# Performance work log

Hardware: AMD Instinct MI355X
Metric: run time of the kernel (lower is better)

The kernel has to match this reference:

```python
import jax, jax.numpy as jnp
import numpy as np

EPS = 1e-12  # torch F.normalize default eps


def _nn_idx(q, ref):
    # q: [P,3], ref: [M,3] -> nearest-ref index per query point (brute-force chamfer NN)
    d = (jnp.sum(q * q, axis=-1, keepdims=True)
         - 2.0 * (q @ ref.T)
         + jnp.sum(ref * ref, axis=-1))  # [P,M]
    return jnp.argmin(d, axis=-1)  # [P]


def _verts_normals(verts, faces):
    # verts: [N,3], faces: [F,3] int. Area-weighted vertex normals (pytorch3d style):
    # accumulate the face cross-product into each incident vertex.
    v0 = verts[faces[:, 0]]
    v1 = verts[faces[:, 1]]
    v2 = verts[faces[:, 2]]
    fn = jnp.cross(v1 - v0, v2 - v0)  # [F,3], magnitude = 2*area
    n = jnp.zeros_like(verts)
    n = n.at[faces[:, 0]].add(fn)
    n = n.at[faces[:, 1]].add(fn)
    n = n.at[faces[:, 2]].add(fn)
    return n  # [N,3] (unnormalized; normalized downstream)


def _normalize(x):
    nrm = jnp.linalg.norm(x, axis=-1, keepdims=True)
    return x / jnp.maximum(nrm, EPS)


def setup_inputs() -> dict:
    key = jax.random.key(0)
    k1, k2, k3, k4 = jax.random.split(key, 4)
    B, P, V, N, F = 8, 2048, 2562, 8192, 16384
    return {
        "pred_points": jax.random.normal(k1, (B, P, 3), dtype=jnp.float32),
        "pred_vertices": jax.random.normal(k2, (B, V, 3), dtype=jnp.float32),
        "gt_vertices": jax.random.normal(k3, (B, N, 3), dtype=jnp.float32),
        "gt_faces": jax.random.randint(k4, (B, F, 3), 0, N, dtype=jnp.int64),
    }


def reference(pred_points, pred_vertices, gt_vertices, gt_faces):
    # nearest gt vertex for every sampled pred point (per-batch chamfer NN)
    nearest_gt_idx = jax.vmap(_nn_idx)(pred_points, gt_vertices)       # [B,P]
    # nearest pred-mesh vertex for every sampled pred point
    nearest_pred_idx = jax.vmap(_nn_idx)(pred_points, pred_vertices)   # [B,P]

    # gather nearest pred vertices: [B,P,3]
    nearest_pred_vertices = jnp.take_along_axis(
        pred_vertices, nearest_pred_idx[..., None], axis=1)

    # gt vertex normals, gathered at nearest gt indices, then normalized
    gt_normals = jax.vmap(_verts_normals)(gt_vertices, gt_faces)       # [B,N,3]
    nearest_gt_normals = jnp.take_along_axis(
        gt_normals, nearest_gt_idx[..., None], axis=1)                 # [B,P,3]
    nearest_gt_normals = _normalize(nearest_gt_normals)

    # edge from nearest pred vertex to sampled point, normalized
    nearest_pred_edges = _normalize(pred_points - nearest_pred_vertices)

    normal_loss = jnp.mean(jnp.abs(
        jnp.sum(nearest_pred_edges * nearest_gt_normals, axis=2)))
    return normal_loss
```

## Files before the change

kernel.cpp:

```cpp
#include <hip/hip_runtime.h>
#include <math.h>

#define BB 8
#define PP 2048
#define VV 2562
#define NV 8192
#define FF 16384
#define EPSF 1e-12f

__global__ __launch_bounds__(256) void face_normals_kernel(
    const float* __restrict__ gtv,
    const int*   __restrict__ faces,
    float*       __restrict__ nrm)
{
    int t = blockIdx.x * blockDim.x + threadIdx.x;
    if (t >= BB * FF) return;
    int b = t / FF;
    const int* fc = faces + (size_t)t * 3;
    int i0 = fc[0], i1 = fc[1], i2 = fc[2];

    const float* vb = gtv + (size_t)b * NV * 3;
    float v0x = vb[i0*3+0], v0y = vb[i0*3+1], v0z = vb[i0*3+2];
    float v1x = vb[i1*3+0], v1y = vb[i1*3+1], v1z = vb[i1*3+2];
    float v2x = vb[i2*3+0], v2y = vb[i2*3+1], v2z = vb[i2*3+2];

    float e1x = v1x - v0x, e1y = v1y - v0y, e1z = v1z - v0z;
    float e2x = v2x - v0x, e2y = v2y - v0y, e2z = v2z - v0z;

    float fnx = e1y * e2z - e1z * e2y;
    float fny = e1z * e2x - e1x * e2z;
    float fnz = e1x * e2y - e1y * e2x;

    float* nb = nrm + (size_t)b * NV * 3;
    atomicAdd(&nb[i0*3+0], fnx); atomicAdd(&nb[i0*3+1], fny); atomicAdd(&nb[i0*3+2], fnz);
    atomicAdd(&nb[i1*3+0], fnx); atomicAdd(&nb[i1*3+1], fny); atomicAdd(&nb[i1*3+2], fnz);
    atomicAdd(&nb[i2*3+0], fnx); atomicAdd(&nb[i2*3+1], fny); atomicAdd(&nb[i2*3+2], fnz);
}

__global__ __launch_bounds__(256) void nn_loss_kernel(
    const float* __restrict__ pp,
    const float* __restrict__ pv,
    const float* __restrict__ gtv,
    const float* __restrict__ nrm,
    float*       __restrict__ partial)
{
    const int lane = threadIdx.x & 63;
    const int wave = threadIdx.x >> 6;
    const int gw   = blockIdx.x * 4 + wave;
    const int b    = gw >> 9;
    const int p0   = (gw & 511) * 4;

    float px[4], py[4], pz[4];
    const float* ppb = pp + ((size_t)b * PP + p0) * 3;
#pragma unroll
    for (int j = 0; j < 4; ++j) {
        px[j] = ppb[j*3+0]; py[j] = ppb[j*3+1]; pz[j] = ppb[j*3+2];
    }

    float bd[4]; int bi[4];
#pragma unroll
    for (int j = 0; j < 4; ++j) { bd[j] = INFINITY; bi[j] = 0; }

    const float* gvb = gtv + (size_t)b * NV * 3;
    for (int i = 0; i < NV / 64; ++i) {
        int r = lane + i * 64;
        float rx = gvb[r*3+0], ry = gvb[r*3+1], rz = gvb[r*3+2];
#pragma unroll
        for (int j = 0; j < 4; ++j) {
            float dx = px[j] - rx, dy = py[j] - ry, dz = pz[j] - rz;
            float d = fmaf(dx, dx, fmaf(dy, dy, dz * dz));
            bool take = d < bd[j];
            bd[j] = take ? d : bd[j];
            bi[j] = take ? r : bi[j];
        }
    }

    int gt_idx[4];
#pragma unroll
    for (int j = 0; j < 4; ++j) {
        float d = bd[j]; int idx = bi[j];
#pragma unroll
        for (int off = 32; off; off >>= 1) {
            float od = __shfl_xor(d, off);
            int   oi = __shfl_xor(idx, off);
            if (od < d || (od == d && oi < idx)) { d = od; idx = oi; }
        }
        gt_idx[j] = idx;
    }

#pragma unroll
    for (int j = 0; j < 4; ++j) { bd[j] = INFINITY; bi[j] = 0; }

    const float* pvb = pv + (size_t)b * VV * 3;
    for (int i = 0; i < (VV + 63) / 64; ++i) {
        int r = lane + i * 64;
        int rc = (r < VV) ? r : (VV - 1);
        float rx = pvb[rc*3+0], ry = pvb[rc*3+1], rz = pvb[rc*3+2];
#pragma unroll
        for (int j = 0; j < 4; ++j) {
            float dx = px[j] - rx, dy = py[j] - ry, dz = pz[j] - rz;
            float d = fmaf(dx, dx, fmaf(dy, dy, dz * dz));
            d = (r < VV) ? d : INFINITY;
            bool take = d < bd[j];
            bd[j] = take ? d : bd[j];
            bi[j] = take ? r : bi[j];
        }
    }

    int pr_idx[4];
#pragma unroll
    for (int j = 0; j < 4; ++j) {
        float d = bd[j]; int idx = bi[j];
#pragma unroll
        for (int off = 32; off; off >>= 1) {
            float od = __shfl_xor(d, off);
            int   oi = __shfl_xor(idx, off);
            if (od < d || (od == d && oi < idx)) { d = od; idx = oi; }
        }
        pr_idx[j] = idx;
    }

    __shared__ float wsum[4];
    if (lane == 0) {
        const float* nb = nrm + (size_t)b * NV * 3;
        float s = 0.f;
#pragma unroll
        for (int j = 0; j < 4; ++j) {
            int vi = pr_idx[j];
            float ex = px[j] - pvb[vi*3+0];
            float ey = py[j] - pvb[vi*3+1];
            float ez = pz[j] - pvb[vi*3+2];
            float el = fmaxf(sqrtf(fmaf(ex, ex, fmaf(ey, ey, ez * ez))), EPSF);

            int ni = gt_idx[j];
            float nx = nb[ni*3+0];
            float ny = nb[ni*3+1];
            float nz = nb[ni*3+2];
            float nl = fmaxf(sqrtf(fmaf(nx, nx, fmaf(ny, ny, nz * nz))), EPSF);

            float dot = fmaf(ex, nx, fmaf(ey, ny, ez * nz));
            s += fabsf(dot / (el * nl));
        }
        wsum[wave] = s;
    }
    __syncthreads();
    if (threadIdx.x == 0)
        partial[blockIdx.x] = wsum[0] + wsum[1] + wsum[2] + wsum[3];
}

__global__ __launch_bounds__(256) void reduce_kernel(
    const float* __restrict__ partial, float* __restrict__ out, int n)
{
    int t = threadIdx.x;
    float s = 0.f;
    for (int i = t; i < n; i += 256) s += partial[i];
#pragma unroll
    for (int off = 32; off; off >>= 1) s += __shfl_xor(s, off);
    __shared__ float ws[4];
    if ((t & 63) == 0) ws[t >> 6] = s;
    __syncthreads();
    if (t == 0) out[0] = (ws[0] + ws[1] + ws[2] + ws[3]) / (float)(BB * PP);
}

extern "C" void kernel_launch(void* const* d_in, const int* in_sizes, int n_in,
                              void* d_out, int out_size, void* d_ws, size_t ws_size,
                              hipStream_t stream) {
    const float* pp    = (const float*)d_in[0];
    const float* pv    = (const float*)d_in[1];
    const float* gtv   = (const float*)d_in[2];
    const int*   faces = (const int*)d_in[3];
    float* out = (float*)d_out;

    float* nrm     = (float*)d_ws;
    float* partial = (float*)((char*)d_ws + (size_t)BB*NV*3*sizeof(float));

    hipMemsetAsync(nrm, 0, (size_t)BB * NV * 3 * sizeof(float), stream);

    face_normals_kernel<<<(BB * FF + 255) / 256, 256, 0, stream>>>(gtv, faces, nrm);

    const int nblocks = (BB * PP) / 16;
    nn_loss_kernel<<<nblocks, 256, 0, stream>>>(pp, pv, gtv, nrm, partial);

    reduce_kernel<<<1, 256, 0, stream>>>(partial, out, nblocks);
}
```

Baseline: 177.8 us.

## Split NN search across two waves per point group and accumulate normals in LDS

The face-normal kernel now runs one 1024-thread block per batch and does its scatter-add into a 96KB shared-memory accumulator before writing out. That replaces the global atomics and the workspace memset, at the cost of using only 8 blocks. The NN kernel splits each reference set into halves handled by paired waves and merges the two results through shared memory. It uses the expanded distance form (rr - 2p·r) to save arithmetic and folds the final reduction into a global atomicAdd, which removes the reduce kernel. The split doubles the number of blocks for the NN search, while the 8-block normals kernel may underuse the GPU.

Result: slower. 294.2 us (+65.5%).

```diff
diff --git a/kernel.cpp b/kernel.cpp
--- a/kernel.cpp
+++ b/kernel.cpp
@@ -7,34 +7,45 @@
 #define NV 8192
 #define FF 16384
 #define EPSF 1e-12f
+#define HNV 4096
+#define HVV 1281
 
-__global__ __launch_bounds__(256) void face_normals_kernel(
+__global__ __launch_bounds__(1024) void face_normals_kernel(
     const float* __restrict__ gtv,
     const int*   __restrict__ faces,
     float*       __restrict__ nrm)
 {
-    int t = blockIdx.x * blockDim.x + threadIdx.x;
-    if (t >= BB * FF) return;
-    int b = t / FF;
-    const int* fc = faces + (size_t)t * 3;
-    int i0 = fc[0], i1 = fc[1], i2 = fc[2];
+    __shared__ float acc[NV * 3];
+    const int b = blockIdx.x;
 
-    const float* vb = gtv + (size_t)b * NV * 3;
-    float v0x = vb[i0*3+0], v0y = vb[i0*3+1], v0z = vb[i0*3+2];
-    float v1x = vb[i1*3+0], v1y = vb[i1*3+1], v1z = vb[i1*3+2];
-    float v2x = vb[i2*3+0], v2y = vb[i2*3+1], v2z = vb[i2*3+2];
+    for (int i = threadIdx.x; i < NV * 3; i += 1024) acc[i] = 0.f;
+    __syncthreads();
 
-    float e1x = v1x - v0x, e1y = v1y - v0y, e1z = v1z - v0z;
-    float e2x = v2x - v0x, e2y = v2y - v0y, e2z = v2z - v0z;
+    const int*   fb = faces + (size_t)b * FF * 3;
+    const float* vb = gtv   + (size_t)b * NV * 3;
 
-    float fnx = e1y * e2z - e1z * e2y;
-    float fny = e1z * e2x - e1x * e2z;
-    float fnz = e1x * e2y - e1y * e2x;
+    for (int f = threadIdx.x; f < FF; f += 1024) {
+        int i0 = fb[f*3+0], i1 = fb[f*3+1], i2 = fb[f*3+2];
+
+        float v0x = vb[i0*3+0], v0y = vb[i0*3+1], v0z = vb[i0*3+2];
+        float v1x = vb[i1*3+0], v1y = vb[i1*3+1], v1z = vb[i1*3+2];
+        float v2x = vb[i2*3+0], v2y = vb[i2*3+1], v2z = vb[i2*3+2];
+
+        float e1x = v1x - v0x, e1y = v1y - v0y, e1z = v1z - v0z;
+        float e2x = v2x - v0x, e2y = v2y - v0y, e2z = v2z - v0z;
+
+        float fnx = e1y * e2z - e1z * e2y;
+        float fny = e1z * e2x - e1x * e2z;
+        float fnz = e1x * e2y - e1y * e2x;
+
+        atomicAdd(&acc[i0*3+0], fnx); atomicAdd(&acc[i0*3+1], fny); atomicAdd(&acc[i0*3+2], fnz);
+        atomicAdd(&acc[i1*3+0], fnx); atomicAdd(&acc[i1*3+1], fny); atomicAdd(&acc[i1*3+2], fnz);
+        atomicAdd(&acc[i2*3+0], fnx); atomicAdd(&acc[i2*3+1], fny); atomicAdd(&acc[i2*3+2], fnz);
+    }
+    __syncthreads();
 
     float* nb = nrm + (size_t)b * NV * 3;
-    atomicAdd(&nb[i0*3+0], fnx); atomicAdd(&nb[i0*3+1], fny); atomicAdd(&nb[i0*3+2], fnz);
-    atomicAdd(&nb[i1*3+0], fnx); atomicAdd(&nb[i1*3+1], fny); atomicAdd(&nb[i1*3+2], fnz);
-    atomicAdd(&nb[i2*3+0], fnx); atomicAdd(&nb[i2*3+1], fny); atomicAdd(&nb[i2*3+2], fnz);
+    for (int i = threadIdx.x; i < NV * 3; i += 1024) nb[i] = acc[i];
 }
 
 __global__ __launch_bounds__(256) void nn_loss_kernel(
@@ -42,40 +53,48 @@
     const float* __restrict__ pv,
     const float* __restrict__ gtv,
     const float* __restrict__ nrm,
-    float*       __restrict__ partial)
+    float*       __restrict__ out)
 {
+    __shared__ float sdg[2][2][4];  __shared__ int sig[2][2][4];
+    __shared__ float sdp[2][2][4];  __shared__ int sip[2][2][4];
+
     const int lane = threadIdx.x & 63;
     const int wave = threadIdx.x >> 6;
-    const int gw   = blockIdx.x * 4 + wave;
-    const int b    = gw >> 9;
-    const int p0   = (gw & 511) * 4;
+    const int g    = wave >> 1;
+    const int h    = wave & 1;
+    const int b    = blockIdx.x >> 8;
+    const int pbase = (blockIdx.x & 255) * 8 + g * 4;
 
-    float px[4], py[4], pz[4];
-    const float* ppb = pp + ((size_t)b * PP + p0) * 3;
+    float m2x[4], m2y[4], m2z[4];
+    {
+        const float* ppb = pp + ((size_t)b * PP + pbase) * 3;
 #pragma unroll
-    for (int j = 0; j < 4; ++j) {
-        px[j] = ppb[j*3+0]; py[j] = ppb[j*3+1]; pz[j] = ppb[j*3+2];
+        for (int j = 0; j < 4; ++j) {
+            m2x[j] = -2.f * ppb[j*3+0];
+            m2y[j] = -2.f * ppb[j*3+1];
+            m2z[j] = -2.f * ppb[j*3+2];
+        }
     }
 
     float bd[4]; int bi[4];
+
 #pragma unroll
     for (int j = 0; j < 4; ++j) { bd[j] = INFINITY; bi[j] = 0; }
-
-    const float* gvb = gtv + (size_t)b * NV * 3;
-    for (int i = 0; i < NV / 64; ++i) {
-        int r = lane + i * 64;
-        float rx = gvb[r*3+0], ry = gvb[r*3+1], rz = gvb[r*3+2];
+    {
+        const float* gvb = gtv + ((size_t)b * NV + (size_t)h * HNV) * 3;
+        for (int i = 0; i < HNV / 64; ++i) {
+            int r = lane + i * 64;
+            float rx = gvb[r*3+0], ry = gvb[r*3+1], rz = gvb[r*3+2];
+            float rr = fmaf(rx, rx, fmaf(ry, ry, rz * rz));
 #pragma unroll
-        for (int j = 0; j < 4; ++j) {
-            float dx = px[j] - rx, dy = py[j] - ry, dz = pz[j] - rz;
-            float d = fmaf(dx, dx, fmaf(dy, dy, dz * dz));
-            bool take = d < bd[j];
-            bd[j] = take ? d : bd[j];
-            bi[j] = take ? r : bi[j];
+            for (int j = 0; j < 4; ++j) {
+                float s = fmaf(m2x[j], rx, fmaf(m2y[j], ry, fmaf(m2z[j], rz, rr)));
+                bool take = s < bd[j];
+                bd[j] = take ? s : bd[j];
+                bi[j] = take ? r : bi[j];
+            }
         }
     }
-
-    int gt_idx[4];
 #pragma unroll
     for (int j = 0; j < 4; ++j) {
         float d = bd[j]; int idx = bi[j];
@@ -85,29 +104,29 @@
             int   oi = __shfl_xor(idx, off);
             if (od < d || (od == d && oi < idx)) { d = od; idx = oi; }
         }
-        gt_idx[j] = idx;
+        if (lane == 0) { sdg[g][h][j] = d; sig[g][h][j] = idx + h * HNV; }
     }
 
 #pragma unroll
     for (int j = 0; j < 4; ++j) { bd[j] = INFINITY; bi[j] = 0; }
-
-    const float* pvb = pv + (size_t)b * VV * 3;
-    for (int i = 0; i < (VV + 63) / 64; ++i) {
-        int r = lane + i * 64;
-        int rc = (r < VV) ? r : (VV - 1);
-        float rx = pvb[rc*3+0], ry = pvb[rc*3+1], rz = pvb[rc*3+2];
+    {
+        const float* pvh = pv + ((size_t)b * VV + (size_t)h * HVV) * 3;
+        for (int i = 0; i < (HVV + 63) / 64; ++i) {
+            int r = lane + i * 64;
+            bool ok = r < HVV;
+            int rc = ok ? r : 0;
+            float rx = pvh[rc*3+0], ry = pvh[rc*3+1], rz = pvh[rc*3+2];
+            float rr = fmaf(rx, rx, fmaf(ry, ry, rz * rz));
 #pragma unroll
-        for (int j = 0; j < 4; ++j) {
-            float dx = px[j] - rx, dy = py[j] - ry, dz = pz[j] - rz;
-            float d = fmaf(dx, dx, fmaf(dy, dy, dz * dz));
-            d = (r < VV) ? d : INFINITY;
-            bool take = d < bd[j];
-            bd[j] = take ? d : bd[j];
-            bi[j] = take ? r : bi[j];
+            for (int j = 0; j < 4; ++j) {
+                float s = fmaf(m2x[j], rx, fmaf(m2y[j], ry, fmaf(m2z[j], rz, rr)));
+                s = ok ? s : INFINITY;
+                bool take = s < bd[j];
+                bd[j] = take ? s : bd[j];
+                bi[j] = take ? r : bi[j];
+            }
         }
     }
-
-    int pr_idx[4];
 #pragma unroll
     for (int j = 0; j < 4; ++j) {
         float d = bd[j]; int idx = bi[j];
@@ -117,49 +136,45 @@
             int   oi = __shfl_xor(idx, off);
             if (od < d || (od == d && oi < idx)) { d = od; idx = oi; }
         }
-        pr_idx[j] = idx;
+        if (lane == 0) { sdp[g][h][j] = d; sip[g][h][j] = idx + h * HVV; }
     }
 
-    __shared__ float wsum[4];
-    if (lane == 0) {
-        const float* nb = nrm + (size_t)b * NV * 3;
+    __syncthreads();
+
+    if (wave == 0) {
         float s = 0.f;
-#pragma unroll
-        for (int j = 0; j < 4; ++j) {
-            int vi = pr_idx[j];
-            float ex = px[j] - pvb[vi*3+0];
-            float ey = py[j] - pvb[vi*3+1];
-            float ez = pz[j] - pvb[vi*3+2];
+        if (lane < 8) {
+            int gg = lane >> 2, q = lane & 3;
+
+            float d0 = sdg[gg][0][q], d1 = sdg[gg][1][q];
+            int   i0 = sig[gg][0][q], i1 = sig[gg][1][q];
+            int gi = (d1 < d0 || (d1 == d0 && i1 < i0)) ? i1 : i0;
+
+            float e0 = sdp[gg][0][q], e1 = sdp[gg][1][q];
+            int   j0 = sip[gg][0][q], j1 = sip[gg][1][q];
+            int pi = (e1 < e0 || (e1 == e0 && j1 < j0)) ? j1 : j0;
+
+            int pidx = (blockIdx.x & 255) * 8 + lane;
+            const float* pq = pp + ((size_t)b * PP + pidx) * 3;
+            float px = pq[0], py = pq[1], pz = pq[2];
+
+            const float* pvr = pv + ((size_t)b * VV + pi) * 3;
+            float ex = px - pvr[0], ey = py - pvr[1], ez = pz - pvr[2];
             float el = fmaxf(sqrtf(fmaf(ex, ex, fmaf(ey, ey, ez * ez))), EPSF);
 
-            int ni = gt_idx[j];
-            float nx = nb[ni*3+0];
-            float ny = nb[ni*3+1];
-            float nz = nb[ni*3+2];
+            const float* nb = nrm + ((size_t)b * NV + gi) * 3;
+            float nx = nb[0], ny = nb[1], nz = nb[2];
             float nl = fmaxf(sqrtf(fmaf(nx, nx, fmaf(ny, ny, nz * nz))), EPSF);
 
             float dot = fmaf(ex, nx, fmaf(ey, ny, ez * nz));
-            s += fabsf(dot / (el * nl));
+            s = fabsf(dot) / (el * nl);
         }
-        wsum[wave] = s;
+        s += __shfl_xor(s, 1);
+        s += __shfl_xor(s, 2);
+        s += __shfl_xor(s, 4);
+        if (lane == 0)
+            atomicAdd(out, s * (1.f / (float)(BB * PP)));
     }
-    __syncthreads();
-    if (threadIdx.x == 0)
-        partial[blockIdx.x] = wsum[0] + wsum[1] + wsum[2] + wsum[3];
-}
-
-__global__ __launch_bounds__(256) void reduce_kernel(
-    const float* __restrict__ partial, float* __restrict__ out, int n)
-{
-    int t = threadIdx.x;
-    float s = 0.f;
-    for (int i = t; i < n; i += 256) s += partial[i];
-#pragma unroll
-    for (int off = 32; off; off >>= 1) s += __shfl_xor(s, off);
-    __shared__ float ws[4];
-    if ((t & 63) == 0) ws[t >> 6] = s;
-    __syncthreads();
-    if (t == 0) out[0] = (ws[0] + ws[1] + ws[2] + ws[3]) / (float)(BB * PP);
 }
 
 extern "C" void kernel_launch(void* const* d_in, const int* in_sizes, int n_in,
@@ -171,15 +186,11 @@
     const int*   faces = (const int*)d_in[3];
     float* out = (float*)d_out;
 
-    float* nrm     = (float*)d_ws;
-    float* partial = (float*)((char*)d_ws + (size_t)BB*NV*3*sizeof(float));
+    float* nrm = (float*)d_ws;
 
-    hipMemsetAsync(nrm, 0, (size_t)BB * NV * 3 * sizeof(float), stream);
+    hipMemsetAsync(out, 0, sizeof(float), stream);
 
-    face_normals_kernel<<<(BB * FF + 255) / 256, 256, 0, stream>>>(gtv, faces, nrm);
+    face_normals_kernel<<<BB, 1024, 0, stream>>>(gtv, faces, nrm);
 
-    const int nblocks = (BB * PP) / 16;
-    nn_loss_kernel<<<nblocks, 256, 0, stream>>>(pp, pv, gtv, nrm, partial);
-
-    reduce_kernel<<<1, 256, 0, stream>>>(partial, out, nblocks);
+    nn_loss_kernel<<<(BB * PP) / 8, 256, 0, stream>>>(pp, pv, gtv, nrm, out);
 }
```

## Expand NN distance, accumulate normals in LDS, fold reduce into atomic

Applied to the files above, without the earlier changes.

The nearest-neighbour loop now ranks candidates by |r|^2 - 2 p·r, precomputed per reference point. This cuts per-pair arithmetic to three FMAs. Face normals are accumulated per batch slice in shared memory before one global atomic pass. The final reduction kernel is replaced by a global atomicAdd, with the output zeroed by memset. The expanded distance can change argmin choices on near ties, and the normals kernel now runs only 32 large blocks.

Result: faster. 162.9 us (-8.4%).

```diff
diff --git a/kernel.cpp b/kernel.cpp
--- a/kernel.cpp
+++ b/kernel.cpp
@@ -7,34 +7,46 @@
 #define NV 8192
 #define FF 16384
 #define EPSF 1e-12f
+#define NSLICE 4
+#define FSLICE (FF / NSLICE)
 
-__global__ __launch_bounds__(256) void face_normals_kernel(
+__global__ __launch_bounds__(1024) void face_normals_kernel(
     const float* __restrict__ gtv,
     const int*   __restrict__ faces,
     float*       __restrict__ nrm)
 {
-    int t = blockIdx.x * blockDim.x + threadIdx.x;
-    if (t >= BB * FF) return;
-    int b = t / FF;
-    const int* fc = faces + (size_t)t * 3;
-    int i0 = fc[0], i1 = fc[1], i2 = fc[2];
+    __shared__ float acc[NV * 3];
+    const int b = blockIdx.x >> 2;
+    const int s = blockIdx.x & 3;
 
-    const float* vb = gtv + (size_t)b * NV * 3;
-    float v0x = vb[i0*3+0], v0y = vb[i0*3+1], v0z = vb[i0*3+2];
-    float v1x = vb[i1*3+0], v1y = vb[i1*3+1], v1z = vb[i1*3+2];
-    float v2x = vb[i2*3+0], v2y = vb[i2*3+1], v2z = vb[i2*3+2];
+    for (int i = threadIdx.x; i < NV * 3; i += 1024) acc[i] = 0.f;
+    __syncthreads();
 
-    float e1x = v1x - v0x, e1y = v1y - v0y, e1z = v1z - v0z;
-    float e2x = v2x - v0x, e2y = v2y - v0y, e2z = v2z - v0z;
+    const int*   fb = faces + ((size_t)b * FF + (size_t)s * FSLICE) * 3;
+    const float* vb = gtv   + (size_t)b * NV * 3;
 
-    float fnx = e1y * e2z - e1z * e2y;
-    float fny = e1z * e2x - e1x * e2z;
-    float fnz = e1x * e2y - e1y * e2x;
+    for (int f = threadIdx.x; f < FSLICE; f += 1024) {
+        int i0 = fb[f*3+0], i1 = fb[f*3+1], i2 = fb[f*3+2];
+
+        float v0x = vb[i0*3+0], v0y = vb[i0*3+1], v0z = vb[i0*3+2];
+        float v1x = vb[i1*3+0], v1y = vb[i1*3+1], v1z = vb[i1*3+2];
+        float v2x = vb[i2*3+0], v2y = vb[i2*3+1], v2z = vb[i2*3+2];
+
+        float e1x = v1x - v0x, e1y = v1y - v0y, e1z = v1z - v0z;
+        float e2x = v2x - v0x, e2y = v2y - v0y, e2z = v2z - v0z;
+
+        float fnx = e1y * e2z - e1z * e2y;
+        float fny = e1z * e2x - e1x * e2z;
+        float fnz = e1x * e2y - e1y * e2x;
+
+        atomicAdd(&acc[i0*3+0], fnx); atomicAdd(&acc[i0*3+1], fny); atomicAdd(&acc[i0*3+2], fnz);
+        atomicAdd(&acc[i1*3+0], fnx); atomicAdd(&acc[i1*3+1], fny); atomicAdd(&acc[i1*3+2], fnz);
+        atomicAdd(&acc[i2*3+0], fnx); atomicAdd(&acc[i2*3+1], fny); atomicAdd(&acc[i2*3+2], fnz);
+    }
+    __syncthreads();
 
     float* nb = nrm + (size_t)b * NV * 3;
-    atomicAdd(&nb[i0*3+0], fnx); atomicAdd(&nb[i0*3+1], fny); atomicAdd(&nb[i0*3+2], fnz);
-    atomicAdd(&nb[i1*3+0], fnx); atomicAdd(&nb[i1*3+1], fny); atomicAdd(&nb[i1*3+2], fnz);
-    atomicAdd(&nb[i2*3+0], fnx); atomicAdd(&nb[i2*3+1], fny); atomicAdd(&nb[i2*3+2], fnz);
+    for (int i = threadIdx.x; i < NV * 3; i += 1024) atomicAdd(&nb[i], acc[i]);
 }
 
 __global__ __launch_bounds__(256) void nn_loss_kernel(
@@ -42,7 +54,7 @@
     const float* __restrict__ pv,
     const float* __restrict__ gtv,
     const float* __restrict__ nrm,
-    float*       __restrict__ partial)
+    float*       __restrict__ out)
 {
     const int lane = threadIdx.x & 63;
     const int wave = threadIdx.x >> 6;
@@ -50,31 +62,31 @@
     const int b    = gw >> 9;
     const int p0   = (gw & 511) * 4;
 
-    float px[4], py[4], pz[4];
+    float px[4], py[4], pz[4], m2x[4], m2y[4], m2z[4];
     const float* ppb = pp + ((size_t)b * PP + p0) * 3;
 #pragma unroll
     for (int j = 0; j < 4; ++j) {
         px[j] = ppb[j*3+0]; py[j] = ppb[j*3+1]; pz[j] = ppb[j*3+2];
+        m2x[j] = -2.f * px[j]; m2y[j] = -2.f * py[j]; m2z[j] = -2.f * pz[j];
     }
 
     float bd[4]; int bi[4];
+
 #pragma unroll
     for (int j = 0; j < 4; ++j) { bd[j] = INFINITY; bi[j] = 0; }
-
     const float* gvb = gtv + (size_t)b * NV * 3;
     for (int i = 0; i < NV / 64; ++i) {
         int r = lane + i * 64;
         float rx = gvb[r*3+0], ry = gvb[r*3+1], rz = gvb[r*3+2];
+        float rr = fmaf(rx, rx, fmaf(ry, ry, rz * rz));
 #pragma unroll
         for (int j = 0; j < 4; ++j) {
-            float dx = px[j] - rx, dy = py[j] - ry, dz = pz[j] - rz;
-            float d = fmaf(dx, dx, fmaf(dy, dy, dz * dz));
-            bool take = d < bd[j];
-            bd[j] = take ? d : bd[j];
+            float s = fmaf(m2x[j], rx, fmaf(m2y[j], ry, fmaf(m2z[j], rz, rr)));
+            bool take = s < bd[j];
+            bd[j] = take ? s : bd[j];
             bi[j] = take ? r : bi[j];
         }
     }
-
     int gt_idx[4];
 #pragma unroll
     for (int j = 0; j < 4; ++j) {
@@ -90,23 +102,22 @@
 
 #pragma unroll
     for (int j = 0; j < 4; ++j) { bd[j] = INFINITY; bi[j] = 0; }
-
     const float* pvb = pv + (size_t)b * VV * 3;
     for (int i = 0; i < (VV + 63) / 64; ++i) {
         int r = lane + i * 64;
-        int rc = (r < VV) ? r : (VV - 1);
+        bool ok = r < VV;
+        int rc = ok ? r : 0;
         float rx = pvb[rc*3+0], ry = pvb[rc*3+1], rz = pvb[rc*3+2];
+        float rr = fmaf(rx, rx, fmaf(ry, ry, rz * rz));
 #pragma unroll
         for (int j = 0; j < 4; ++j) {
-            float dx = px[j] - rx, dy = py[j] - ry, dz = pz[j] - rz;
-            float d = fmaf(dx, dx, fmaf(dy, dy, dz * dz));
-            d = (r < VV) ? d : INFINITY;
-            bool take = d < bd[j];
-            bd[j] = take ? d : bd[j];
+            float s = fmaf(m2x[j], rx, fmaf(m2y[j], ry, fmaf(m2z[j], rz, rr)));
+            s = ok ? s : INFINITY;
+            bool take = s < bd[j];
+            bd[j] = take ? s : bd[j];
             bi[j] = take ? r : bi[j];
         }
     }
-
     int pr_idx[4];
 #pragma unroll
     for (int j = 0; j < 4; ++j) {
@@ -139,27 +150,14 @@
             float nl = fmaxf(sqrtf(fmaf(nx, nx, fmaf(ny, ny, nz * nz))), EPSF);
 
             float dot = fmaf(ex, nx, fmaf(ey, ny, ez * nz));
-            s += fabsf(dot / (el * nl));
+            s += fabsf(dot) / (el * nl);
         }
         wsum[wave] = s;
     }
     __syncthreads();
     if (threadIdx.x == 0)
-        partial[blockIdx.x] = wsum[0] + wsum[1] + wsum[2] + wsum[3];
-}
-
-__global__ __launch_bounds__(256) void reduce_kernel(
-    const float* __restrict__ partial, float* __restrict__ out, int n)
-{
-    int t = threadIdx.x;
-    float s = 0.f;
-    for (int i = t; i < n; i += 256) s += partial[i];
-#pragma unroll
-    for (int off = 32; off; off >>= 1) s += __shfl_xor(s, off);
-    __shared__ float ws[4];
-    if ((t & 63) == 0) ws[t >> 6] = s;
-    __syncthreads();
-    if (t == 0) out[0] = (ws[0] + ws[1] + ws[2] + ws[3]) / (float)(BB * PP);
+        atomicAdd(out, (wsum[0] + wsum[1] + wsum[2] + wsum[3]) *
+                       (1.f / (float)(BB * PP)));
 }
 
 extern "C" void kernel_launch(void* const* d_in, const int* in_sizes, int n_in,
@@ -171,15 +169,12 @@
     const int*   faces = (const int*)d_in[3];
     float* out = (float*)d_out;
 
-    float* nrm     = (float*)d_ws;
-    float* partial = (float*)((char*)d_ws + (size_t)BB*NV*3*sizeof(float));
+    float* nrm = (float*)d_ws;
 
     hipMemsetAsync(nrm, 0, (size_t)BB * NV * 3 * sizeof(float), stream);
+    hipMemsetAsync(out, 0, sizeof(float), stream);
 
-    face_normals_kernel<<<(BB * FF + 255) / 256, 256, 0, stream>>>(gtv, faces, nrm);
+    face_normals_kernel<<<BB * NSLICE, 1024, 0, stream>>>(gtv, faces, nrm);
 
-    const int nblocks = (BB * PP) / 16;
-    nn_loss_kernel<<<nblocks, 256, 0, stream>>>(pp, pv, gtv, nrm, partial);
-
-    reduce_kernel<<<1, 256, 0, stream>>>(partial, out, nblocks);
+    nn_loss_kernel<<<(BB * PP) / 16, 256, 0, stream>>>(pp, pv, gtv, nrm, out);
 }
```
